# Kernel optimization log

Hardware: AMD Instinct MI355X
Metric: run time of the kernel (lower is better)

Reference implementation:

```python
import jax, jax.numpy as jnp
import numpy as np
import math

B, S, D = 2, 2048, 1024
H = 16
HD = D // H
W = 128


def setup_inputs() -> dict:
    key = jax.random.key(0)
    ks = jax.random.split(key, 5)
    scale = 1.0 / math.sqrt(D)
    return {
        "x": jax.random.normal(ks[0], (B, S, D), dtype=jnp.float32),
        "in_proj_w": jax.random.normal(ks[1], (3 * D, D), dtype=jnp.float32) * scale,
        "in_proj_b": jax.random.normal(ks[2], (3 * D,), dtype=jnp.float32) * 0.02,
        "out_proj_w": jax.random.normal(ks[3], (D, D), dtype=jnp.float32) * scale,
        "out_proj_b": jax.random.normal(ks[4], (D,), dtype=jnp.float32) * 0.02,
        "window_size": W,
    }


def reference(x, in_proj_w, in_proj_b, out_proj_w, out_proj_b, window_size):
    b, s, d = x.shape
    # Combined qkv projection, as nn.MultiheadAttention does
    qkv = x @ in_proj_w.T + in_proj_b  # [B,S,3D]
    q, k, v = jnp.split(qkv, 3, axis=-1)
    # [B,H,S,HD]
    def heads(t):
        return t.reshape(b, s, H, HD).transpose(0, 2, 1, 3)
    q, k, v = heads(q), heads(k), heads(v)
    scale = 1.0 / math.sqrt(HD)
    scores = jnp.einsum("bhqd,bhkd->bhqk", q, k) * scale  # [B,H,S,S]
    # banded sliding-window mask: disallow |i-j| > window_size
    i = jnp.arange(s)[:, None]
    j = jnp.arange(s)[None, :]
    banned = jnp.abs(i - j) > window_size  # [S,S] bool
    scores = jnp.where(banned[None, None], -jnp.inf, scores)
    attn = jax.nn.softmax(scores, axis=-1)
    out = jnp.einsum("bhqk,bhkd->bhqd", attn, v)  # [B,H,S,HD]
    out = out.transpose(0, 2, 1, 3).reshape(b, s, d)
    return out @ out_proj_w.T + out_proj_b
```

## Files before the change

### kernel.cpp

```cpp
#include <hip/hip_runtime.h>

#define S_LEN 2048
#define DMODEL 1024
#define NHEAD 16
#define HDIM 64

typedef __bf16 bf16x8 __attribute__((ext_vector_type(8)));
typedef float f32x4 __attribute__((ext_vector_type(4)));

typedef __attribute__((address_space(1))) const void gconst_void;
typedef __attribute__((address_space(3))) void lds_void;

__device__ __forceinline__ unsigned short f2bf(float f) {
    unsigned u = __builtin_bit_cast(unsigned, f);
    u += 0x7fffu + ((u >> 16) & 1u);
    return (unsigned short)(u >> 16);
}

#define N4_X  (2 * S_LEN * DMODEL / 4)
#define N4_W1 (3 * DMODEL * DMODEL / 4)
#define N4_W2 (DMODEL * DMODEL / 4)
__global__ __launch_bounds__(256) void cvt_all(const float* __restrict__ x,
                                               const float* __restrict__ w1,
                                               const float* __restrict__ w2,
                                               unsigned short* __restrict__ xb,
                                               unsigned short* __restrict__ w1b,
                                               unsigned short* __restrict__ w2b) {
    int i = blockIdx.x * 256 + threadIdx.x;
    const float* s;
    unsigned short* d;
    int off;
    if (i < N4_X)            { s = x;  d = xb;  off = i; }
    else if (i < N4_X + N4_W1) { s = w1; d = w1b; off = i - N4_X; }
    else if (i < N4_X + N4_W1 + N4_W2) { s = w2; d = w2b; off = i - N4_X - N4_W1; }
    else return;
    float4 f = ((const float4*)s)[off];
    ushort4 o;
    o.x = f2bf(f.x); o.y = f2bf(f.y); o.z = f2bf(f.z); o.w = f2bf(f.w);
    ((ushort4*)d)[off] = o;
}

__global__ __launch_bounds__(256) void gemm_qkv(const unsigned short* __restrict__ A,
                                                const unsigned short* __restrict__ Bt,
                                                const float* __restrict__ bias,
                                                unsigned short* __restrict__ qk,
                                                unsigned short* __restrict__ vT,
                                                int M, int N, int K) {
    __shared__ unsigned short lds[(64 + 128) * 64] __attribute__((aligned(16)));
    unsigned short* lA = lds;
    unsigned short* lB = lds + 64 * 64;

    const int tid  = threadIdx.x;
    const int lane = tid & 63;
    const int w    = tid >> 6;
    const int quad = lane >> 4;
    const int l16  = lane & 15;

    const int m0 = blockIdx.x * 64;
    const int n0 = blockIdx.y * 128;

    const int rowi = tid >> 3;
    const int csw  = ((tid & 7) ^ (rowi & 7)) * 8;
    const unsigned short* aSrc = A + (size_t)(m0 + rowi) * K + csw;
    const unsigned short* bSrc = Bt + (size_t)(n0 + rowi) * K + csw;
    const int dstOff = (w * 8) * 64;

    f32x4 acc[2][4];
    {
        f32x4 z = {0.f, 0.f, 0.f, 0.f};
        #pragma unroll
        for (int i = 0; i < 2; i++)
            #pragma unroll
            for (int j = 0; j < 4; j++) acc[i][j] = z;
    }

    const int wm = (w & 1) * 32;
    const int wn = (w >> 1) * 64;

    for (int kt = 0; kt < K; kt += 64) {
        __syncthreads();
        #pragma unroll
        for (int p = 0; p < 2; p++) {
            __builtin_amdgcn_global_load_lds(
                (gconst_void*)(aSrc + (size_t)p * 32 * K + kt),
                (lds_void*)(&lA[dstOff + p * 32 * 64]), 16, 0, 0);
        }
        #pragma unroll
        for (int p = 0; p < 4; p++) {
            __builtin_amdgcn_global_load_lds(
                (gconst_void*)(bSrc + (size_t)p * 32 * K + kt),
                (lds_void*)(&lB[dstOff + p * 32 * 64]), 16, 0, 0);
        }
        __syncthreads();

        #pragma unroll
        for (int kk = 0; kk < 2; kk++) {
            bf16x8 af[2], bfr[4];
            const int xsw = ((kk * 4 + quad) ^ (l16 & 7)) * 8;
            #pragma unroll
            for (int t = 0; t < 2; t++)
                af[t] = *(const bf16x8*)&lA[(wm + t * 16 + l16) * 64 + xsw];
            #pragma unroll
            for (int t = 0; t < 4; t++)
                bfr[t] = *(const bf16x8*)&lB[(wn + t * 16 + l16) * 64 + xsw];
            #pragma unroll
            for (int i = 0; i < 2; i++)
                #pragma unroll
                for (int j = 0; j < 4; j++)
                    acc[i][j] = __builtin_amdgcn_mfma_f32_16x16x32_bf16(af[i], bfr[j], acc[i][j], 0, 0, 0);
        }
    }

    if (n0 < 2 * DMODEL) {
        #pragma unroll
        for (int j = 0; j < 4; j++) {
            const int n = n0 + wn + j * 16 + l16;
            const float bv = bias[n];
            const float scl = (n < DMODEL) ? 0.125f : 1.0f;
            #pragma unroll
            for (int i = 0; i < 2; i++) {
                const int mrow = m0 + wm + i * 16 + quad * 4;
                #pragma unroll
                for (int r = 0; r < 4; r++) {
                    float v = (acc[i][j][r] + bv) * scl;
                    qk[(size_t)(mrow + r) * 2048 + n] = f2bf(v);
                }
            }
        }
    } else {
        __syncthreads();
        unsigned short* T = lds;
        #pragma unroll
        for (int j = 0; j < 4; j++) {
            const int nl = wn + j * 16 + l16;
            const float bv = bias[n0 + nl];
            #pragma unroll
            for (int i = 0; i < 2; i++) {
                const int ml0 = wm + i * 16 + quad * 4;
                ushort4 pk;
                pk.x = f2bf(acc[i][j][0] + bv);
                pk.y = f2bf(acc[i][j][1] + bv);
                pk.z = f2bf(acc[i][j][2] + bv);
                pk.w = f2bf(acc[i][j][3] + bv);
                const int addr = nl * 64 + (((ml0 >> 3) ^ (nl & 7)) << 3) + (ml0 & 7);
                *(ushort4*)&T[addr] = pk;
            }
        }
        __syncthreads();
        const int b   = m0 >> 11;
        const int sg  = m0 & (S_LEN - 1);
        const int hd0 = n0 - 2 * DMODEL;
        const int c   = tid & 7;
        #pragma unroll
        for (int pass = 0; pass < 4; pass++) {
            const int dl = (tid >> 3) + pass * 32;
            bf16x8 val = *(const bf16x8*)&T[dl * 64 + ((c ^ (dl & 7)) << 3)];
            *(bf16x8*)&vT[(size_t)(b * DMODEL + hd0 + dl) * S_LEN + sg + c * 8] = val;
        }
    }
}

__global__ __launch_bounds__(256) void gemm_out(const unsigned short* __restrict__ A,
                                                const unsigned short* __restrict__ Bt,
                                                const float* __restrict__ bias,
                                                float* __restrict__ out,
                                                int M, int N, int K) {
    __shared__ unsigned short lA[64 * 64] __attribute__((aligned(16)));
    __shared__ unsigned short lB[128 * 64] __attribute__((aligned(16)));

    const int tid  = threadIdx.x;
    const int lane = tid & 63;
    const int w    = tid >> 6;
    const int quad = lane >> 4;
    const int l16  = lane & 15;

    const int m0 = blockIdx.x * 64;
    const int n0 = blockIdx.y * 128;

    const int rowi = tid >> 3;
    const int csw  = ((tid & 7) ^ (rowi & 7)) * 8;
    const unsigned short* aSrc = A + (size_t)(m0 + rowi) * K + csw;
    const unsigned short* bSrc = Bt + (size_t)(n0 + rowi) * K + csw;
    const int dstOff = (w * 8) * 64;

    f32x4 acc[2][4];
    {
        f32x4 z = {0.f, 0.f, 0.f, 0.f};
        #pragma unroll
        for (int i = 0; i < 2; i++)
            #pragma unroll
            for (int j = 0; j < 4; j++) acc[i][j] = z;
    }

    const int wm = (w & 1) * 32;
    const int wn = (w >> 1) * 64;

    for (int kt = 0; kt < K; kt += 64) {
        __syncthreads();
        #pragma unroll
        for (int p = 0; p < 2; p++) {
            __builtin_amdgcn_global_load_lds(
                (gconst_void*)(aSrc + (size_t)p * 32 * K + kt),
                (lds_void*)(&lA[dstOff + p * 32 * 64]), 16, 0, 0);
        }
        #pragma unroll
        for (int p = 0; p < 4; p++) {
            __builtin_amdgcn_global_load_lds(
                (gconst_void*)(bSrc + (size_t)p * 32 * K + kt),
                (lds_void*)(&lB[dstOff + p * 32 * 64]), 16, 0, 0);
        }
        __syncthreads();

        #pragma unroll
        for (int kk = 0; kk < 2; kk++) {
            bf16x8 af[2], bfr[4];
            const int xsw = ((kk * 4 + quad) ^ (l16 & 7)) * 8;
            #pragma unroll
            for (int t = 0; t < 2; t++)
                af[t] = *(const bf16x8*)&lA[(wm + t * 16 + l16) * 64 + xsw];
            #pragma unroll
            for (int t = 0; t < 4; t++)
                bfr[t] = *(const bf16x8*)&lB[(wn + t * 16 + l16) * 64 + xsw];
            #pragma unroll
            for (int i = 0; i < 2; i++)
                #pragma unroll
                for (int j = 0; j < 4; j++)
                    acc[i][j] = __builtin_amdgcn_mfma_f32_16x16x32_bf16(af[i], bfr[j], acc[i][j], 0, 0, 0);
        }
    }

    #pragma unroll
    for (int j = 0; j < 4; j++) {
        const int n = n0 + wn + j * 16 + l16;
        const float bv = bias[n];
        #pragma unroll
        for (int i = 0; i < 2; i++) {
            const int mrow = m0 + wm + i * 16 + quad * 4;
            #pragma unroll
            for (int r = 0; r < 4; r++)
                out[(size_t)(mrow + r) * N + n] = acc[i][j][r] + bv;
        }
    }
}

__global__ __launch_bounds__(256) void attn_win(const unsigned short* __restrict__ qk,
                                                const unsigned short* __restrict__ vT,
                                                unsigned short* __restrict__ attnout,
                                                const int* __restrict__ wptr) {
    __shared__ unsigned short lK[64 * 64] __attribute__((aligned(16)));
    __shared__ unsigned short lV[64 * 64] __attribute__((aligned(16)));
    __shared__ unsigned short lP[4][16 * 64] __attribute__((aligned(16)));

    const int W = wptr[0];
    const int tid  = threadIdx.x;
    const int lane = tid & 63;
    const int w    = tid >> 6;
    const int quad = lane >> 4;
    const int l16  = lane & 15;

    const int q0 = blockIdx.x * 64;
    const int h  = blockIdx.y;
    const size_t rowbase = (size_t)blockIdx.z * S_LEN;

    const int qrow = q0 + w * 16 + l16;
    bf16x8 qf0, qf1;
    {
        const unsigned short* qp = qk + (rowbase + qrow) * (2 * DMODEL) + h * HDIM;
        qf0 = *(const bf16x8*)(qp + quad * 8);
        qf1 = *(const bf16x8*)(qp + 32 + quad * 8);
    }

    const unsigned short* kbasep = qk + rowbase * (2 * DMODEL) + DMODEL + h * HDIM;
    const unsigned short* vbase  = vT + (size_t)(blockIdx.z * DMODEL + h * HDIM) * S_LEN;

    f32x4 o[4];
    { f32x4 z = {0.f,0.f,0.f,0.f}; o[0]=z; o[1]=z; o[2]=z; o[3]=z; }
    float lsum[4] = {0.f, 0.f, 0.f, 0.f};

    const int iq = q0 + w * 16 + quad * 4;
    int lo[4], hi[4];
    #pragma unroll
    for (int r = 0; r < 4; r++) {
        const int i = iq + r;
        lo[r] = max(i - W, 0);
        hi[r] = min(i + W, S_LEN - 1);
    }

    const int kbase = q0 - W;
    const int nch = (2 * W + 64 + 63) >> 6;

    const int skey = tid >> 3;
    const int sch  = tid & 7;
    const unsigned short* ldsKdst = &lK[(size_t)w * 512];
    const unsigned short* ldsVdst = &lV[(size_t)w * 512];

    for (int c = 0; c < nch; c++) {
        const int kc0 = kbase + c * 64;
        if (kc0 >= S_LEN || kc0 + 63 < 0) continue;

        __syncthreads();
        #pragma unroll
        for (int p = 0; p < 2; p++) {
            const int row = p * 32 + skey;
            const int cs  = sch ^ (row & 7);
            int kg = kc0 + row;
            kg = kg < 0 ? 0 : (kg > S_LEN - 1 ? S_LEN - 1 : kg);
            __builtin_amdgcn_global_load_lds(
                (gconst_void*)(kbasep + (size_t)kg * (2 * DMODEL) + cs * 8),
                (lds_void*)(ldsKdst + p * 2048), 16, 0, 0);
            int s0a = kc0 + cs * 8;
            s0a = s0a < 0 ? 0 : (s0a > S_LEN - 8 ? S_LEN - 8 : s0a);
            __builtin_amdgcn_global_load_lds(
                (gconst_void*)(vbase + (size_t)row * S_LEN + s0a),
                (lds_void*)(ldsVdst + p * 2048), 16, 0, 0);
        }
        __syncthreads();

        f32x4 s4[4];
        { f32x4 z = {0.f,0.f,0.f,0.f}; s4[0]=z; s4[1]=z; s4[2]=z; s4[3]=z; }
        #pragma unroll
        for (int half = 0; half < 2; half++) {
            const bf16x8 qf = half ? qf1 : qf0;
            const int cs = half * 4 + quad;
            #pragma unroll
            for (int kt = 0; kt < 4; kt++) {
                const int key = kt * 16 + l16;
                bf16x8 kf = *(const bf16x8*)&lK[key * 64 + ((cs ^ (key & 7)) << 3)];
                s4[kt] = __builtin_amdgcn_mfma_f32_16x16x32_bf16(qf, kf, s4[kt], 0, 0, 0);
            }
        }

        const bool fullvalid = (kc0 >= 0) && (kc0 + 63 < S_LEN) &&
                               (kc0 >= q0 + 63 - W) && (kc0 + 63 <= q0 + W);
        #pragma unroll
        for (int r = 0; r < 4; r++) {
            const int q = quad * 4 + r;
            const int qsw = q & 7;
            float ps = 0.f;
            #pragma unroll
            for (int kt = 0; kt < 4; kt++) {
                float p;
                if (fullvalid) {
                    p = __expf(s4[kt][r]);
                } else {
                    const int j = kc0 + kt * 16 + l16;
                    const bool v = (j >= lo[r]) && (j <= hi[r]);
                    p = v ? __expf(s4[kt][r]) : 0.f;
                }
                ps += p;
                const int ct = kt * 2 + (l16 >> 3);
                lP[w][q * 64 + ((ct ^ qsw) << 3) + (l16 & 7)] = f2bf(p);
            }
            lsum[r] += ps;
        }

        __builtin_amdgcn_s_waitcnt(0xc07f);

        #pragma unroll
        for (int ks = 0; ks < 2; ks++) {
            const int cs = ks * 4 + quad;
            bf16x8 pf = *(const bf16x8*)&lP[w][l16 * 64 + ((cs ^ (l16 & 7)) << 3)];
            #pragma unroll
            for (int dt = 0; dt < 4; dt++) {
                const int d = dt * 16 + l16;
                bf16x8 vf = *(const bf16x8*)&lV[d * 64 + ((cs ^ (d & 7)) << 3)];
                o[dt] = __builtin_amdgcn_mfma_f32_16x16x32_bf16(pf, vf, o[dt], 0, 0, 0);
            }
        }
    }

    #pragma unroll
    for (int r = 0; r < 4; r++) {
        float l = lsum[r];
        l += __shfl_xor(l, 1);
        l += __shfl_xor(l, 2);
        l += __shfl_xor(l, 4);
        l += __shfl_xor(l, 8);
        const float inv = 1.f / l;
        #pragma unroll
        for (int t = 0; t < 4; t++) {
            attnout[(rowbase + iq + r) * DMODEL + h * HDIM + t * 16 + l16] = f2bf(o[t][r] * inv);
        }
    }
}

extern "C" void kernel_launch(void* const* d_in, const int* in_sizes, int n_in,
                              void* d_out, int out_size, void* d_ws, size_t ws_size,
                              hipStream_t stream) {
    const float* x   = (const float*)d_in[0];
    const float* w1  = (const float*)d_in[1];
    const float* b1  = (const float*)d_in[2];
    const float* w2  = (const float*)d_in[3];
    const float* b2  = (const float*)d_in[4];
    const int* wsz   = (const int*)d_in[5];

    char* ws = (char*)d_ws;
    unsigned short* xb    = (unsigned short*)(ws);
    unsigned short* attnb = (unsigned short*)(ws);
    unsigned short* w1b   = (unsigned short*)(ws + (8u << 20));
    unsigned short* w2b   = (unsigned short*)(ws + (14u << 20));
    unsigned short* qkb   = (unsigned short*)(ws + (16u << 20));
    unsigned short* vTb   = (unsigned short*)(ws + (32u << 20));

    const int M = 2 * S_LEN;

    cvt_all<<<(N4_X + N4_W1 + N4_W2 + 255) / 256, 256, 0, stream>>>(x, w1, w2, xb, w1b, w2b);

    gemm_qkv<<<dim3(M / 64, 3 * DMODEL / 128), 256, 0, stream>>>(xb, w1b, b1, qkb, vTb, M, 3 * DMODEL, DMODEL);

    attn_win<<<dim3(S_LEN / 64, NHEAD, 2), 256, 0, stream>>>(qkb, vTb, attnb, wsz);

    gemm_out<<<dim3(M / 64, DMODEL / 128), 256, 0, stream>>>(attnb, w2b, b2, (float*)d_out, M, DMODEL, DMODEL);
}
```

Before: 157.5 us.

## Double-buffer K/V tiles in windowed attention and shrink output GEMM N-tile

The attention kernel now keeps two LDS buffers for K and V. It prefetches the next 64-key chunk while the current chunk runs through QK^T, softmax and PV, so global-to-LDS latency is meant to hide behind the MFMA work. It also computes the valid chunk range up front instead of skipping chunks inside the loop. Separately, the output projection GEMM tile goes from 64x128 to 64x64, which doubles the block count to improve occupancy and CU coverage, at the cost of more A-tile reloads and less reuse per block.

```diff
diff --git a/kernel.cpp b/kernel.cpp
--- a/kernel.cpp
+++ b/kernel.cpp
@@ -166,7 +166,7 @@
                                                 float* __restrict__ out,
                                                 int M, int N, int K) {
     __shared__ unsigned short lA[64 * 64] __attribute__((aligned(16)));
-    __shared__ unsigned short lB[128 * 64] __attribute__((aligned(16)));
+    __shared__ unsigned short lB[64 * 64] __attribute__((aligned(16)));
 
     const int tid  = threadIdx.x;
     const int lane = tid & 63;
@@ -175,7 +175,7 @@
     const int l16  = lane & 15;
 
     const int m0 = blockIdx.x * 64;
-    const int n0 = blockIdx.y * 128;
+    const int n0 = blockIdx.y * 64;
 
     const int rowi = tid >> 3;
     const int csw  = ((tid & 7) ^ (rowi & 7)) * 8;
@@ -183,17 +183,17 @@
     const unsigned short* bSrc = Bt + (size_t)(n0 + rowi) * K + csw;
     const int dstOff = (w * 8) * 64;
 
-    f32x4 acc[2][4];
+    f32x4 acc[2][2];
     {
         f32x4 z = {0.f, 0.f, 0.f, 0.f};
         #pragma unroll
         for (int i = 0; i < 2; i++)
             #pragma unroll
-            for (int j = 0; j < 4; j++) acc[i][j] = z;
+            for (int j = 0; j < 2; j++) acc[i][j] = z;
     }
 
     const int wm = (w & 1) * 32;
-    const int wn = (w >> 1) * 64;
+    const int wn = (w >> 1) * 32;
 
     for (int kt = 0; kt < K; kt += 64) {
         __syncthreads();
@@ -202,9 +202,6 @@
             __builtin_amdgcn_global_load_lds(
                 (gconst_void*)(aSrc + (size_t)p * 32 * K + kt),
                 (lds_void*)(&lA[dstOff + p * 32 * 64]), 16, 0, 0);
-        }
-        #pragma unroll
-        for (int p = 0; p < 4; p++) {
             __builtin_amdgcn_global_load_lds(
                 (gconst_void*)(bSrc + (size_t)p * 32 * K + kt),
                 (lds_void*)(&lB[dstOff + p * 32 * 64]), 16, 0, 0);
@@ -213,24 +210,23 @@
 
         #pragma unroll
         for (int kk = 0; kk < 2; kk++) {
-            bf16x8 af[2], bfr[4];
+            bf16x8 af[2], bfr[2];
             const int xsw = ((kk * 4 + quad) ^ (l16 & 7)) * 8;
             #pragma unroll
-            for (int t = 0; t < 2; t++)
-                af[t] = *(const bf16x8*)&lA[(wm + t * 16 + l16) * 64 + xsw];
-            #pragma unroll
-            for (int t = 0; t < 4; t++)
+            for (int t = 0; t < 2; t++) {
+                af[t]  = *(const bf16x8*)&lA[(wm + t * 16 + l16) * 64 + xsw];
                 bfr[t] = *(const bf16x8*)&lB[(wn + t * 16 + l16) * 64 + xsw];
+            }
             #pragma unroll
             for (int i = 0; i < 2; i++)
                 #pragma unroll
-                for (int j = 0; j < 4; j++)
+                for (int j = 0; j < 2; j++)
                     acc[i][j] = __builtin_amdgcn_mfma_f32_16x16x32_bf16(af[i], bfr[j], acc[i][j], 0, 0, 0);
         }
     }
 
     #pragma unroll
-    for (int j = 0; j < 4; j++) {
+    for (int j = 0; j < 2; j++) {
         const int n = n0 + wn + j * 16 + l16;
         const float bv = bias[n];
         #pragma unroll
@@ -247,8 +243,8 @@
                                                 const unsigned short* __restrict__ vT,
                                                 unsigned short* __restrict__ attnout,
                                                 const int* __restrict__ wptr) {
-    __shared__ unsigned short lK[64 * 64] __attribute__((aligned(16)));
-    __shared__ unsigned short lV[64 * 64] __attribute__((aligned(16)));
+    __shared__ unsigned short lK[2][64 * 64] __attribute__((aligned(16)));
+    __shared__ unsigned short lV[2][64 * 64] __attribute__((aligned(16)));
     __shared__ unsigned short lP[4][16 * 64] __attribute__((aligned(16)));
 
     const int W = wptr[0];
@@ -288,17 +284,13 @@
 
     const int kbase = q0 - W;
     const int nch = (2 * W + 64 + 63) >> 6;
+    const int c_start = (kbase < 0) ? ((-kbase) >> 6) : 0;
+    const int c_end   = min(nch, ((S_LEN - 1 - kbase) >> 6) + 1);
 
     const int skey = tid >> 3;
     const int sch  = tid & 7;
-    const unsigned short* ldsKdst = &lK[(size_t)w * 512];
-    const unsigned short* ldsVdst = &lV[(size_t)w * 512];
-
-    for (int c = 0; c < nch; c++) {
-        const int kc0 = kbase + c * 64;
-        if (kc0 >= S_LEN || kc0 + 63 < 0) continue;
-
-        __syncthreads();
+
+    auto stage = [&](int buf, int kc0) {
         #pragma unroll
         for (int p = 0; p < 2; p++) {
             const int row = p * 32 + skey;
@@ -307,14 +299,23 @@
             kg = kg < 0 ? 0 : (kg > S_LEN - 1 ? S_LEN - 1 : kg);
             __builtin_amdgcn_global_load_lds(
                 (gconst_void*)(kbasep + (size_t)kg * (2 * DMODEL) + cs * 8),
-                (lds_void*)(ldsKdst + p * 2048), 16, 0, 0);
+                (lds_void*)(&lK[buf][w * 512 + p * 2048]), 16, 0, 0);
             int s0a = kc0 + cs * 8;
             s0a = s0a < 0 ? 0 : (s0a > S_LEN - 8 ? S_LEN - 8 : s0a);
             __builtin_amdgcn_global_load_lds(
                 (gconst_void*)(vbase + (size_t)row * S_LEN + s0a),
-                (lds_void*)(ldsVdst + p * 2048), 16, 0, 0);
-        }
-        __syncthreads();
+                (lds_void*)(&lV[buf][w * 512 + p * 2048]), 16, 0, 0);
+        }
+    };
+
+    stage(c_start & 1, kbase + c_start * 64);
+
+    for (int c = c_start; c < c_end; c++) {
+        const int kc0 = kbase + c * 64;
+        const int buf = c & 1;
+
+        __syncthreads();
+        if (c + 1 < c_end) stage(buf ^ 1, kc0 + 64);
 
         f32x4 s4[4];
         { f32x4 z = {0.f,0.f,0.f,0.f}; s4[0]=z; s4[1]=z; s4[2]=z; s4[3]=z; }
@@ -325,7 +326,7 @@
             #pragma unroll
             for (int kt = 0; kt < 4; kt++) {
                 const int key = kt * 16 + l16;
-                bf16x8 kf = *(const bf16x8*)&lK[key * 64 + ((cs ^ (key & 7)) << 3)];
+                bf16x8 kf = *(const bf16x8*)&lK[buf][key * 64 + ((cs ^ (key & 7)) << 3)];
                 s4[kt] = __builtin_amdgcn_mfma_f32_16x16x32_bf16(qf, kf, s4[kt], 0, 0, 0);
             }
         }
@@ -363,7 +364,7 @@
             #pragma unroll
             for (int dt = 0; dt < 4; dt++) {
                 const int d = dt * 16 + l16;
-                bf16x8 vf = *(const bf16x8*)&lV[d * 64 + ((cs ^ (d & 7)) << 3)];
+                bf16x8 vf = *(const bf16x8*)&lV[buf][d * 64 + ((cs ^ (d & 7)) << 3)];
                 o[dt] = __builtin_amdgcn_mfma_f32_16x16x32_bf16(pf, vf, o[dt], 0, 0, 0);
             }
         }
@@ -410,5 +411,5 @@
 
     attn_win<<<dim3(S_LEN / 64, NHEAD, 2), 256, 0, stream>>>(qkb, vTb, attnb, wsz);
 
-    gemm_out<<<dim3(M / 64, DMODEL / 128), 256, 0, stream>>>(attnb, w2b, b2, (float*)d_out, M, DMODEL, DMODEL);
-}
+    gemm_out<<<dim3(M / 64, DMODEL / 64), 256, 0, stream>>>(attnb, w2b, b2, (float*)d_out, M, DMODEL, DMODEL);
+}
```

After: 156.5 us. No clear change (-0.6%).
